# Optimization experiments

Measured on AMD Instinct MI355X. Metric: run time of the kernel, lower is better.

The kernel has to match this reference:

```python
import jax, jax.numpy as jnp
import numpy as np

EPS = 1e-6
H = 16
CHUNK = 128

def _fmap(x):
    # elu(x) + 1 positive feature map
    return jax.nn.elu(x) + 1.0

def _causal_lin_attn(Qf, Kf, V, eps):
    # Math-identical chunkwise form of the cumsum causal linear attention.
    B, Hh, N, D = Qf.shape
    Dv = V.shape[-1]
    nc = N // CHUNK
    qs = jnp.moveaxis(Qf.reshape(B, Hh, nc, CHUNK, D), 2, 0)
    ks = jnp.moveaxis(Kf.reshape(B, Hh, nc, CHUNK, D), 2, 0)
    vs = jnp.moveaxis(V.reshape(B, Hh, nc, CHUNK, Dv), 2, 0)
    mask = jnp.tril(jnp.ones((CHUNK, CHUNK), dtype=bool))  # inclusive causal within chunk
    S0 = jnp.zeros((B, Hh, D, Dv), Qf.dtype)
    z0 = jnp.zeros((B, Hh, D), Qf.dtype)

    def step(carry, xs):
        S, z = carry
        q, k, v = xs  # (B,H,C,D), (B,H,C,D), (B,H,C,Dv)
        A = jnp.einsum('bhqd,bhkd->bhqk', q, k)
        A = jnp.where(mask, A, 0.0)
        num = jnp.einsum('bhqd,bhdv->bhqv', q, S) + jnp.einsum('bhqk,bhkv->bhqv', A, v)
        den = jnp.einsum('bhqd,bhd->bhq', q, z) + A.sum(-1)
        out = num / (den[..., None] + eps)
        S = S + jnp.einsum('bhkd,bhkv->bhdv', k, v)
        z = z + k.sum(2)
        return (S, z), out

    _, out = jax.lax.scan(step, (S0, z0), (qs, ks, vs))
    return jnp.moveaxis(out, 0, 2).reshape(B, Hh, N, Dv)

def _mhla(Q, K, V, Wq, Wk, Wv, Wo, causal):
    B, N, E = Q.shape
    D = E // H
    q = (Q @ Wq.T).reshape(B, N, H, D).transpose(0, 2, 1, 3)  # (B,H,N,D)
    k = (K @ Wk.T).reshape(B, N, H, D).transpose(0, 2, 1, 3)
    v = (V @ Wv.T).reshape(B, N, H, D).transpose(0, 2, 1, 3)
    Qf, Kf = _fmap(q), _fmap(k)
    if causal:
        out = _causal_lin_attn(Qf, Kf, v, EPS)
    else:
        KV = jnp.einsum('bhnd,bhnv->bhdv', Kf, v)
        ksum = Kf.sum(2)
        num = jnp.einsum('bhnd,bhdv->bhnv', Qf, KV)
        den = jnp.einsum('bhnd,bhd->bhn', Qf, ksum)[..., None]
        out = num / (den + EPS)
    out = out.transpose(0, 2, 1, 3).reshape(B, N, E)
    return out @ Wo.T

def setup_inputs():
    key = jax.random.key(0)
    ks = jax.random.split(key, 7)
    B, N, E = 2, 2048, 1024

    def xavier(k, shape):
        lim = (6.0 / (shape[0] + shape[1])) ** 0.5
        return jax.random.uniform(k, shape, jnp.float32, -lim, lim)

    return {
        'Q': jax.random.normal(ks[0], (B, N, E), jnp.float32),
        'K': jax.random.normal(ks[1], (B, N, E), jnp.float32),
        'V': jax.random.normal(ks[2], (B, N, E), jnp.float32),
        'Wq': xavier(ks[3], (E, E)),
        'Wk': xavier(ks[4], (E, E)),
        'Wv': xavier(ks[5], (E, E)),
        'Wo': xavier(ks[6], (E, E)),
        'causal': 1,
    }

def reference(Q, K, V, Wq, Wk, Wv, Wo, causal):
    return _mhla(Q, K, V, Wq, Wk, Wv, Wo, causal)
```

## Files before the change

kernel.cpp:

```cpp
#include <hip/hip_runtime.h>
#include <hip/hip_bf16.h>
#include <stdint.h>

#define B_   2
#define N_   2048
#define E_   1024
#define H_   16
#define D_   64
#define CH_  128
#define NC_  16
#define BH_  32
#define M_   4096
#define K_   1024
#define EPS_F 1e-6f

typedef __attribute__((ext_vector_type(8))) __bf16 bf16x8;
typedef __attribute__((ext_vector_type(4))) float  f32x4;

static __device__ __forceinline__ f32x4 mfma16(bf16x8 a, bf16x8 b, f32x4 c) {
  return __builtin_amdgcn_mfma_f32_16x16x32_bf16(a, b, c, 0, 0, 0);
}

static __device__ __forceinline__ unsigned short f2bf(float f) {
  union { float fv; unsigned int u; } x; x.fv = f;
  unsigned int r = x.u + 0x7FFFu + ((x.u >> 16) & 1u);
  return (unsigned short)(r >> 16);
}
static __device__ __forceinline__ float fmap(float x) {
  return x > 0.f ? (x + 1.f) : __expf(x);
}
static __device__ __forceinline__ void gload16(const void* g, void* l) {
  __builtin_amdgcn_global_load_lds(
      (const __attribute__((address_space(1))) void*)g,
      (__attribute__((address_space(3))) void*)l, 16, 0, 0);
}

__global__ __launch_bounds__(256)
void conv_kernel(const float* __restrict__ Q, const float* __restrict__ Kx,
                 const float* __restrict__ V, const float* __restrict__ Wq,
                 const float* __restrict__ Wk, const float* __restrict__ Wv,
                 const float* __restrict__ Wo,
                 unsigned short* __restrict__ Xb, unsigned short* __restrict__ Wb) {
  int gid = blockIdx.x * 256 + threadIdx.x;
  int idx = gid * 4;
  const float* src; unsigned short* dst; int off;
  if (idx < (3 << 22)) {
    int which = idx >> 22;
    off = idx & ((1 << 22) - 1);
    src = (which == 0) ? Q : (which == 1) ? Kx : V;
    dst = Xb + ((size_t)which << 22);
  } else {
    int j = idx - (3 << 22);
    int which = j >> 20;
    off = j & ((1 << 20) - 1);
    src = (which == 0) ? Wq : (which == 1) ? Wk : (which == 2) ? Wv : Wo;
    dst = Wb + ((size_t)which << 20);
  }
  float4 v = *(const float4*)(src + off);
  ushort4 o;
  o.x = f2bf(v.x); o.y = f2bf(v.y); o.z = f2bf(v.z); o.w = f2bf(v.w);
  *(ushort4*)(dst + off) = o;
}

template<int MODE>
__global__ __launch_bounds__(256)
void gemm_kernel(const unsigned short* __restrict__ Aall,
                 const unsigned short* __restrict__ Wall,
                 unsigned short* __restrict__ qf,
                 unsigned short* __restrict__ kf,
                 unsigned short* __restrict__ kt,
                 unsigned short* __restrict__ vt,
                 float* __restrict__ outf) {
  constexpr int BM = (MODE == 0) ? 128 : 64;
  constexpr int WM = BM / 32;
  constexpr int NWG = (MODE == 0) ? 768 : 512;
  __shared__ __align__(16) unsigned short As[2][BM * 32];
  __shared__ __align__(16) unsigned short Bs[2][128 * 32];

  const int wg = (blockIdx.x & 7) * (NWG >> 3) + (blockIdx.x >> 3);
  const int nb = wg & 7;
  const int mb = (MODE == 0) ? ((wg >> 3) & 31) : (wg >> 3);
  const int z  = (MODE == 0) ? (wg >> 8) : 3;

  const unsigned short* Ag = Aall + ((MODE == 0) ? ((size_t)z << 22) : 0);
  const unsigned short* Bg = Wall + ((size_t)z << 20);
  const int tid = threadIdx.x;
  const int w = tid >> 6, l = tid & 63;
  const int wm = w >> 1, wn = w & 1;
  const int fl = l & 15, fh = l >> 4;
  const int lrow = l >> 2, lc8 = l & 3;

  const unsigned short* gA = Ag + (size_t)(mb * BM + w * (BM / 4) + lrow) * K_ + lc8 * 8;
  const unsigned short* gB = Bg + (size_t)(nb * 128 + w * 32 + lrow) * K_ + lc8 * 8;

  f32x4 acc[WM][4] = {};

  auto stage = [&](int k0, int buf) {
    unsigned short* lA = &As[buf][w * (BM / 4) * 32];
    unsigned short* lB = &Bs[buf][w * 32 * 32];
    gload16(gA + k0, lA);
    if (MODE == 0) gload16(gA + k0 + 16 * K_, lA + 512);
    gload16(gB + k0, lB);
    gload16(gB + k0 + 16 * K_, lB + 512);
  };

  stage(0, 0);
  __syncthreads();
  int cur = 0;
  for (int t = 0; t < K_ / 32; ++t) {
    if (t + 1 < K_ / 32) stage((t + 1) * 32, cur ^ 1);
    bf16x8 av[WM], bv[4];
#pragma unroll
    for (int i = 0; i < WM; i++)
      av[i] = *(const bf16x8*)(&As[cur][(wm * (BM / 2) + i * 16 + fl) * 32 + fh * 8]);
#pragma unroll
    for (int j = 0; j < 4; j++)
      bv[j] = *(const bf16x8*)(&Bs[cur][(wn * 64 + j * 16 + fl) * 32 + fh * 8]);
#pragma unroll
    for (int i = 0; i < WM; i++)
#pragma unroll
      for (int j = 0; j < 4; j++)
        acc[i][j] = mfma16(av[i], bv[j], acc[i][j]);
    __syncthreads();
    cur ^= 1;
  }

#pragma unroll
  for (int i = 0; i < WM; i++)
#pragma unroll
    for (int j = 0; j < 4; j++)
#pragma unroll
      for (int r = 0; r < 4; r++) {
        int m = mb * BM + wm * (BM / 2) + i * 16 + fh * 4 + r;
        int e = nb * 128 + wn * 64 + j * 16 + fl;
        float v = acc[i][j][r];
        if (MODE == 1) {
          outf[(size_t)m * E_ + e] = v;
        } else {
          int b = m >> 11, n = m & (N_ - 1), h = e >> 6, d = e & 63;
          int bh = b * H_ + h;
          if (z == 0) {
            qf[((size_t)bh * N_ + n) * D_ + d] = f2bf(fmap(v));
          } else if (z == 1) {
            unsigned short s = f2bf(fmap(v));
            kf[((size_t)bh * N_ + n) * D_ + d] = s;
            kt[((size_t)bh * D_ + d) * N_ + n] = s;
          } else {
            vt[((size_t)bh * D_ + d) * N_ + n] = f2bf(v);
          }
        }
      }
}

__global__ __launch_bounds__(64)
void chunkkv_kernel(const unsigned short* __restrict__ kt,
                    const unsigned short* __restrict__ vt,
                    float* __restrict__ Sc, float* __restrict__ zc) {
  const int bh = blockIdx.x, c = blockIdx.y;
  const int l = threadIdx.x;
  const int fl = l & 15, fh = l >> 4;
  const int n0 = c * CH_;
  const unsigned short* ktb = kt + (size_t)bh * D_ * N_;
  const unsigned short* vtb = vt + (size_t)bh * D_ * N_;
  f32x4 acc[4][4] = {};
#pragma unroll
  for (int ks = 0; ks < 4; ks++) {
    bf16x8 av[4], bv[4];
#pragma unroll
    for (int i = 0; i < 4; i++)
      av[i] = *(const bf16x8*)(ktb + (size_t)(i * 16 + fl) * N_ + n0 + ks * 32 + fh * 8);
#pragma unroll
    for (int j = 0; j < 4; j++)
      bv[j] = *(const bf16x8*)(vtb + (size_t)(j * 16 + fl) * N_ + n0 + ks * 32 + fh * 8);
#pragma unroll
    for (int i = 0; i < 4; i++)
#pragma unroll
      for (int j = 0; j < 4; j++)
        acc[i][j] = mfma16(av[i], bv[j], acc[i][j]);
  }
  float* Scb = Sc + ((size_t)(bh * NC_ + c) << 12);
#pragma unroll
  for (int i = 0; i < 4; i++)
#pragma unroll
    for (int j = 0; j < 4; j++)
#pragma unroll
      for (int r = 0; r < 4; r++)
        Scb[(i * 16 + fh * 4 + r) * 64 + j * 16 + fl] = acc[i][j][r];
  float s = 0.f;
  const unsigned short* kr = ktb + (size_t)l * N_ + n0;
#pragma unroll
  for (int t = 0; t < 16; t++) {
    bf16x8 v8 = *(const bf16x8*)(kr + t * 8);
#pragma unroll
    for (int e = 0; e < 8; e++) s += (float)v8[e];
  }
  zc[(bh * NC_ + c) * 64 + l] = s;
}

__global__ __launch_bounds__(256)
void prefix_kernel(const float* __restrict__ Sc, const float* __restrict__ zc,
                   unsigned short* __restrict__ St, float* __restrict__ zx) {
  int gid = blockIdx.x * 256 + threadIdx.x;
  if (blockIdx.x < 512) {
    int bh = gid >> 12;
    int idx = gid & 4095;
    int d = idx >> 6, dv = idx & 63;
    float s = 0.f;
    for (int c = 0; c < NC_; c++) {
      size_t base = ((size_t)(bh * NC_ + c)) << 12;
      St[base + (dv << 6) + d] = f2bf(s);
      s += Sc[base + idx];
    }
  } else {
    int j = gid - 512 * 256;
    int bh = j >> 6, d = j & 63;
    float s = 0.f;
    for (int c = 0; c < NC_; c++) {
      zx[(bh * NC_ + c) * 64 + d] = s;
      s += zc[(bh * NC_ + c) * 64 + d];
    }
  }
}

__global__ __launch_bounds__(256)
void attn_kernel(const unsigned short* __restrict__ qf,
                 const unsigned short* __restrict__ kf,
                 const unsigned short* __restrict__ vt,
                 const unsigned short* __restrict__ St,
                 const float* __restrict__ zx,
                 unsigned short* __restrict__ AO) {
  __shared__ __align__(16) unsigned short A_lds[128 * 136];
  __shared__ float den_s[128];
  const int c = blockIdx.x, bh = blockIdx.y;
  const int tid = threadIdx.x, w = tid >> 6, l = tid & 63;
  const int fl = l & 15, fh = l >> 4;
  const int n0 = c * CH_;
  const unsigned short* qfb = qf + ((size_t)bh * N_ + n0) * D_;
  const unsigned short* kfb = kf + ((size_t)bh * N_ + n0) * D_;
  const unsigned short* vtb = vt + (size_t)bh * D_ * N_;
  const unsigned short* Stb = St + (((size_t)(bh * NC_ + c)) << 12);
  const float* zxb = zx + (bh * NC_ + c) * 64;

  f32x4 accA[2][8] = {};
#pragma unroll
  for (int ks = 0; ks < 2; ks++) {
    bf16x8 av[2], bv[8];
#pragma unroll
    for (int i = 0; i < 2; i++)
      av[i] = *(const bf16x8*)(qfb + (size_t)(w * 32 + i * 16 + fl) * D_ + ks * 32 + fh * 8);
#pragma unroll
    for (int j = 0; j < 8; j++)
      bv[j] = *(const bf16x8*)(kfb + (size_t)(j * 16 + fl) * D_ + ks * 32 + fh * 8);
#pragma unroll
    for (int i = 0; i < 2; i++)
#pragma unroll
      for (int j = 0; j < 8; j++)
        accA[i][j] = mfma16(av[i], bv[j], accA[i][j]);
  }
#pragma unroll
  for (int i = 0; i < 2; i++)
#pragma unroll
    for (int j = 0; j < 8; j++)
#pragma unroll
      for (int r = 0; r < 4; r++) {
        int qrow = w * 32 + i * 16 + fh * 4 + r;
        int kcol = j * 16 + fl;
        float v = (kcol <= qrow) ? accA[i][j][r] : 0.f;
        A_lds[qrow * 136 + kcol] = f2bf(v);
      }
  __syncthreads();

  if (tid < 128) {
    int row = tid;
    float dq = 0.f;
    const unsigned short* qr = qfb + (size_t)row * D_;
#pragma unroll
    for (int t = 0; t < 8; t++) {
      bf16x8 q8 = *(const bf16x8*)(qr + t * 8);
#pragma unroll
      for (int e = 0; e < 8; e++) dq += (float)q8[e] * zxb[t * 8 + e];
    }
    float ds = 0.f;
#pragma unroll
    for (int t = 0; t < 16; t++) {
      bf16x8 a8 = *(const bf16x8*)(A_lds + row * 136 + t * 8);
#pragma unroll
      for (int e = 0; e < 8; e++) ds += (float)a8[e];
    }
    den_s[row] = dq + ds + EPS_F;
  }
  __syncthreads();

  f32x4 accO[2][4] = {};
#pragma unroll
  for (int ks = 0; ks < 2; ks++) {
    bf16x8 av[2], bv[4];
#pragma unroll
    for (int i = 0; i < 2; i++)
      av[i] = *(const bf16x8*)(qfb + (size_t)(w * 32 + i * 16 + fl) * D_ + ks * 32 + fh * 8);
#pragma unroll
    for (int j = 0; j < 4; j++)
      bv[j] = *(const bf16x8*)(Stb + (j * 16 + fl) * 64 + ks * 32 + fh * 8);
#pragma unroll
    for (int i = 0; i < 2; i++)
#pragma unroll
      for (int j = 0; j < 4; j++)
        accO[i][j] = mfma16(av[i], bv[j], accO[i][j]);
  }
#pragma unroll
  for (int ks = 0; ks < 4; ks++) {
    bf16x8 av[2], bv[4];
#pragma unroll
    for (int i = 0; i < 2; i++)
      av[i] = *(const bf16x8*)(A_lds + (w * 32 + i * 16 + fl) * 136 + ks * 32 + fh * 8);
#pragma unroll
    for (int j = 0; j < 4; j++)
      bv[j] = *(const bf16x8*)(vtb + (size_t)(j * 16 + fl) * N_ + n0 + ks * 32 + fh * 8);
#pragma unroll
    for (int i = 0; i < 2; i++)
#pragma unroll
      for (int j = 0; j < 4; j++)
        accO[i][j] = mfma16(av[i], bv[j], accO[i][j]);
  }

  const int b = bh >> 4, h = bh & 15;
#pragma unroll
  for (int i = 0; i < 2; i++)
#pragma unroll
    for (int j = 0; j < 4; j++)
#pragma unroll
      for (int r = 0; r < 4; r++) {
        int qrow = w * 32 + i * 16 + fh * 4 + r;
        int dv = j * 16 + fl;
        float o = accO[i][j][r] / den_s[qrow];
        AO[((size_t)(b * N_ + n0 + qrow)) * E_ + h * 64 + dv] = f2bf(o);
      }
}

extern "C" void kernel_launch(void* const* d_in, const int* in_sizes, int n_in,
                              void* d_out, int out_size, void* d_ws, size_t ws_size,
                              hipStream_t stream) {
  const float* Q  = (const float*)d_in[0];
  const float* Kx = (const float*)d_in[1];
  const float* V  = (const float*)d_in[2];
  const float* Wq = (const float*)d_in[3];
  const float* Wk = (const float*)d_in[4];
  const float* Wv = (const float*)d_in[5];
  const float* Wo = (const float*)d_in[6];

  char* p = (char*)d_ws;
  unsigned short* Xb = (unsigned short*)p; p += (size_t)3 * M_ * K_ * 2;
  unsigned short* Wb = (unsigned short*)p; p += (size_t)4 * E_ * E_ * 2;
  unsigned short* qf = (unsigned short*)p; p += (size_t)BH_ * N_ * D_ * 2;
  unsigned short* kf = (unsigned short*)p; p += (size_t)BH_ * N_ * D_ * 2;
  unsigned short* kt = (unsigned short*)p; p += (size_t)BH_ * N_ * D_ * 2;
  unsigned short* vt = (unsigned short*)p; p += (size_t)BH_ * N_ * D_ * 2;
  float*          Sc = (float*)p;          p += (size_t)BH_ * NC_ * D_ * D_ * 4;
  float*          zc = (float*)p;          p += (size_t)BH_ * NC_ * D_ * 4;
  unsigned short* St = (unsigned short*)p; p += (size_t)BH_ * NC_ * D_ * D_ * 2;
  float*          zx = (float*)p;          p += (size_t)BH_ * NC_ * D_ * 4;
  unsigned short* AO = (unsigned short*)p; p += (size_t)M_ * E_ * 2;

  conv_kernel<<<dim3(16384), dim3(256), 0, stream>>>(Q, Kx, V, Wq, Wk, Wv, Wo, Xb, Wb);
  gemm_kernel<0><<<dim3(768), dim3(256), 0, stream>>>(Xb, Wb, qf, kf, kt, vt, nullptr);
  chunkkv_kernel<<<dim3(32, 16), dim3(64), 0, stream>>>(kt, vt, Sc, zc);
  prefix_kernel<<<dim3(520), dim3(256), 0, stream>>>(Sc, zc, St, zx);
  attn_kernel<<<dim3(16, 32), dim3(256), 0, stream>>>(qf, kf, vt, St, zx, AO);
  gemm_kernel<1><<<dim3(512), dim3(256), 0, stream>>>(AO, Wb, nullptr, nullptr,
                                                      nullptr, nullptr, (float*)d_out);
}
```

Baseline: 233.1 us.

## Swizzle GEMM LDS layout to single buffer, transpose chunk KV product to avoid strided stores

```diff
diff --git a/kernel.cpp b/kernel.cpp
--- a/kernel.cpp
+++ b/kernel.cpp
@@ -74,8 +74,8 @@
   constexpr int BM = (MODE == 0) ? 128 : 64;
   constexpr int WM = BM / 32;
   constexpr int NWG = (MODE == 0) ? 768 : 512;
-  __shared__ __align__(16) unsigned short As[2][BM * 32];
-  __shared__ __align__(16) unsigned short Bs[2][128 * 32];
+  __shared__ __align__(16) unsigned short As[BM * 32];
+  __shared__ __align__(16) unsigned short Bs[128 * 32];
 
   const int wg = (blockIdx.x & 7) * (NWG >> 3) + (blockIdx.x >> 3);
   const int nb = wg & 7;
@@ -88,41 +88,37 @@
   const int w = tid >> 6, l = tid & 63;
   const int wm = w >> 1, wn = w & 1;
   const int fl = l & 15, fh = l >> 4;
-  const int lrow = l >> 2, lc8 = l & 3;
-
-  const unsigned short* gA = Ag + (size_t)(mb * BM + w * (BM / 4) + lrow) * K_ + lc8 * 8;
-  const unsigned short* gB = Bg + (size_t)(nb * 128 + w * 32 + lrow) * K_ + lc8 * 8;
+  const int lrow = l >> 2;
+  const int swz = (l & 3) ^ ((l >> 3) & 3);
+
+  const unsigned short* gA = Ag + (size_t)(mb * BM + w * (BM / 4) + lrow) * K_ + swz * 8;
+  const unsigned short* gB = Bg + (size_t)(nb * 128 + w * 32 + lrow) * K_ + swz * 8;
+  unsigned short* lA = As + w * (BM / 4) * 32;
+  unsigned short* lB = Bs + w * 1024;
+
+  const int rs = (fh ^ ((fl >> 1) & 3)) * 8;
 
   f32x4 acc[WM][4] = {};
 
-  auto stage = [&](int k0, int buf) {
-    unsigned short* lA = &As[buf][w * (BM / 4) * 32];
-    unsigned short* lB = &Bs[buf][w * 32 * 32];
+  for (int k0 = 0; k0 < K_; k0 += 32) {
+    __syncthreads();
     gload16(gA + k0, lA);
     if (MODE == 0) gload16(gA + k0 + 16 * K_, lA + 512);
     gload16(gB + k0, lB);
     gload16(gB + k0 + 16 * K_, lB + 512);
-  };
-
-  stage(0, 0);
-  __syncthreads();
-  int cur = 0;
-  for (int t = 0; t < K_ / 32; ++t) {
-    if (t + 1 < K_ / 32) stage((t + 1) * 32, cur ^ 1);
+    __syncthreads();
     bf16x8 av[WM], bv[4];
 #pragma unroll
     for (int i = 0; i < WM; i++)
-      av[i] = *(const bf16x8*)(&As[cur][(wm * (BM / 2) + i * 16 + fl) * 32 + fh * 8]);
-#pragma unroll
-    for (int j = 0; j < 4; j++)
-      bv[j] = *(const bf16x8*)(&Bs[cur][(wn * 64 + j * 16 + fl) * 32 + fh * 8]);
+      av[i] = *(const bf16x8*)(As + (wm * (BM / 2) + i * 16 + fl) * 32 + rs);
+#pragma unroll
+    for (int j = 0; j < 4; j++)
+      bv[j] = *(const bf16x8*)(Bs + (wn * 64 + j * 16 + fl) * 32 + rs);
 #pragma unroll
     for (int i = 0; i < WM; i++)
 #pragma unroll
       for (int j = 0; j < 4; j++)
         acc[i][j] = mfma16(av[i], bv[j], acc[i][j]);
-    __syncthreads();
-    cur ^= 1;
   }
 
 #pragma unroll
@@ -168,10 +164,10 @@
     bf16x8 av[4], bv[4];
 #pragma unroll
     for (int i = 0; i < 4; i++)
-      av[i] = *(const bf16x8*)(ktb + (size_t)(i * 16 + fl) * N_ + n0 + ks * 32 + fh * 8);
-#pragma unroll
-    for (int j = 0; j < 4; j++)
-      bv[j] = *(const bf16x8*)(vtb + (size_t)(j * 16 + fl) * N_ + n0 + ks * 32 + fh * 8);
+      av[i] = *(const bf16x8*)(vtb + (size_t)(i * 16 + fl) * N_ + n0 + ks * 32 + fh * 8);
+#pragma unroll
+    for (int j = 0; j < 4; j++)
+      bv[j] = *(const bf16x8*)(ktb + (size_t)(j * 16 + fl) * N_ + n0 + ks * 32 + fh * 8);
 #pragma unroll
     for (int i = 0; i < 4; i++)
 #pragma unroll
@@ -204,11 +200,10 @@
   if (blockIdx.x < 512) {
     int bh = gid >> 12;
     int idx = gid & 4095;
-    int d = idx >> 6, dv = idx & 63;
     float s = 0.f;
     for (int c = 0; c < NC_; c++) {
       size_t base = ((size_t)(bh * NC_ + c)) << 12;
-      St[base + (dv << 6) + d] = f2bf(s);
+      St[base + idx] = f2bf(s);
       s += Sc[base + idx];
     }
   } else {
```

Measured after the change: 214.4 us. 8.0% less time.
